# Kernel optimization log

Measured on AMD Instinct MI355X. Metric: run time of the kernel, lower is better.

The kernel has to match this reference:

```python
import jax, jax.numpy as jnp
import numpy as np

DIM = 768
HEADS = 12
HD = DIM // HEADS  # 64
WIN = 14
N = WIN * WIN  # 196
MLP_HID = 3072
EPS = 1e-6
SCALE = HD ** -0.5


def _ln(x, g, b):
    m = jnp.mean(x, axis=-1, keepdims=True)
    v = jnp.mean(jnp.square(x - m), axis=-1, keepdims=True)
    return (x - m) * jax.lax.rsqrt(v + EPS) * g + b


def _rel_table(rel):
    coords = jnp.arange(WIN)[:, None] - jnp.arange(WIN)[None, :] + (WIN - 1)
    return rel[coords]


def _window_partition(x, ws):
    B, H, W, C = x.shape
    pad_h = (ws - H % ws) % ws
    pad_w = (ws - W % ws) % ws
    x = jnp.pad(x, ((0, 0), (0, pad_h), (0, pad_w), (0, 0)))
    Hp, Wp = H + pad_h, W + pad_w
    x = x.reshape(B, Hp // ws, ws, Wp // ws, ws, C)
    win = x.transpose(0, 1, 3, 2, 4, 5).reshape(-1, ws, ws, C)
    return win, (Hp, Wp)


def _window_unpartition(win, ws, pad_hw, hw):
    Hp, Wp = pad_hw
    H, W = hw
    B = win.shape[0] // (Hp * Wp // ws // ws)
    x = win.reshape(B, Hp // ws, Wp // ws, ws, ws, -1)
    x = x.transpose(0, 1, 3, 2, 4, 5).reshape(B, Hp, Wp, -1)
    return x[:, :H, :W, :]


def _attention(x, qkv_w, qkv_b, proj_w, proj_b, rel_pos_h, rel_pos_w):
    Bw = x.shape[0]
    qkv = x.reshape(Bw, N, DIM) @ qkv_w + qkv_b  # (Bw, N, 3*DIM)
    qkv = qkv.reshape(Bw, N, 3, HEADS, HD).transpose(2, 0, 3, 1, 4)
    qkv = qkv.reshape(3, Bw * HEADS, N, HD)
    q, k, v = qkv[0], qkv[1], qkv[2]
    attn = jnp.einsum('bnd,bmd->bnm', q * SCALE, k)  # (Bw*H, N, N)
    Rh = _rel_table(rel_pos_h)
    Rw = _rel_table(rel_pos_w)
    r_q = q.reshape(-1, WIN, WIN, HD)
    rel_h = jnp.einsum('bhwc,hkc->bhwk', r_q, Rh)
    rel_w = jnp.einsum('bhwc,wkc->bhwk', r_q, Rw)
    attn = (attn.reshape(-1, WIN, WIN, WIN, WIN)
            + rel_h[:, :, :, :, None]
            + rel_w[:, :, :, None, :]).reshape(-1, N, N)
    attn = jax.nn.softmax(attn, axis=-1)
    out = jnp.einsum('bnm,bmd->bnd', attn, v)
    out = out.reshape(Bw, HEADS, WIN, WIN, HD).transpose(0, 2, 3, 1, 4)
    out = out.reshape(Bw, WIN, WIN, DIM)
    return out @ proj_w + proj_b


def setup_inputs() -> dict:
    key = jax.random.key(0)
    ks = jax.random.split(key, 10)
    s = 0.02
    return {
        'x': jax.random.normal(ks[0], (2, 64, 64, DIM), jnp.float32),
        'ln1_g': jnp.ones((DIM,), jnp.float32),
        'ln1_b': jnp.zeros((DIM,), jnp.float32),
        'qkv_w': jax.random.normal(ks[1], (DIM, 3 * DIM), jnp.float32) * s,
        'qkv_b': jax.random.normal(ks[2], (3 * DIM,), jnp.float32) * s,
        'proj_w': jax.random.normal(ks[3], (DIM, DIM), jnp.float32) * s,
        'proj_b': jax.random.normal(ks[4], (DIM,), jnp.float32) * s,
        'rel_pos_h': jax.random.normal(ks[5], (2 * WIN - 1, HD), jnp.float32) * s,
        'rel_pos_w': jax.random.normal(ks[6], (2 * WIN - 1, HD), jnp.float32) * s,
        'ln2_g': jnp.ones((DIM,), jnp.float32),
        'ln2_b': jnp.zeros((DIM,), jnp.float32),
        'fc1_w': jax.random.normal(ks[7], (DIM, MLP_HID), jnp.float32) * s,
        'fc1_b': jnp.zeros((MLP_HID,), jnp.float32),
        'fc2_w': jax.random.normal(ks[8], (MLP_HID, DIM), jnp.float32) * s,
        'fc2_b': jnp.zeros((DIM,), jnp.float32),
    }


def reference(x, ln1_g, ln1_b, qkv_w, qkv_b, proj_w, proj_b,
              rel_pos_h, rel_pos_w, ln2_g, ln2_b, fc1_w, fc1_b, fc2_w, fc2_b):
    B, H, W, _ = x.shape
    shortcut = x
    h = _ln(x, ln1_g, ln1_b)
    win, pad_hw = _window_partition(h, WIN)
    win = _attention(win, qkv_w, qkv_b, proj_w, proj_b, rel_pos_h, rel_pos_w)
    h = _window_unpartition(win, WIN, pad_hw, (H, W))
    x = shortcut + h  # drop_path prob 0 -> identity
    h = _ln(x, ln2_g, ln2_b)
    h = jax.nn.gelu(h @ fc1_w + fc1_b, approximate=False) @ fc2_w + fc2_b
    return x + h
```

## Files before the change

### kernel.cpp

```cpp
#include <hip/hip_runtime.h>
#include <hip/hip_bf16.h>
#include <math.h>


#define DIMC 768
#define HEADS 12
#define WIN 14
#define NTOK 196
#define NWIN 50
#define MROWS 9800
#define YROWS 8192
#define MLP_HID 3072

using bf16x8 = __attribute__((ext_vector_type(8))) short;
using f32x4  = __attribute__((ext_vector_type(4))) float;

__device__ __forceinline__ float bf2f(unsigned short u) {
    return __uint_as_float(((unsigned)u) << 16);
}
__device__ __forceinline__ unsigned short f2bf(float f) {
    unsigned u = __float_as_uint(f);
    unsigned r = (u + 0x7fffu + ((u >> 16) & 1u)) >> 16;
    return (unsigned short)r;
}
__device__ __forceinline__ void gl2lds16(const unsigned short* g, unsigned short* l) {
    __builtin_amdgcn_global_load_lds(
        (const __attribute__((address_space(1))) void*)g,
        (__attribute__((address_space(3))) void*)l, 16, 0, 0);
}

__device__ __forceinline__ float fast_gelu(float v) {
    float u = v * 0.70710678118654752f;
    float a = fabsf(u);
    float t = __builtin_amdgcn_rcpf(fmaf(0.3275911f, a, 1.0f));
    float p = t * fmaf(t, fmaf(t, fmaf(t, fmaf(t, 1.061405429f, -1.453152027f),
                       1.421413741f), -0.284496736f), 0.254829592f);
    float e = __expf(-u * u);
    float er = fmaf(-p, e, 1.0f);
    er = copysignf(er, v);
    return 0.5f * v * (1.0f + er);
}

__global__ __launch_bounds__(256) void transpose_all(
        const float* __restrict__ Wq, unsigned short* __restrict__ Tq,
        const float* __restrict__ Wp, unsigned short* __restrict__ Tp,
        const float* __restrict__ W1, unsigned short* __restrict__ T1,
        const float* __restrict__ W2, unsigned short* __restrict__ T2) {
    int id = blockIdx.x;
    const float* W; unsigned short* Wt; int K, N, nbx, rel;
    if (id < 432)       { W = Wq; Wt = Tq; K = 768;  N = 2304; nbx = 36; rel = id; }
    else if (id < 576)  { W = Wp; Wt = Tp; K = 768;  N = 768;  nbx = 12; rel = id - 432; }
    else if (id < 1152) { W = W1; Wt = T1; K = 768;  N = 3072; nbx = 48; rel = id - 576; }
    else                { W = W2; Wt = T2; K = 3072; N = 768;  nbx = 12; rel = id - 1152; }
    int bx = rel % nbx, by = rel / nbx;
    __shared__ float t[64][65];
    int k0 = by << 6, n0 = bx << 6;
    int tn = threadIdx.x & 63;
    int tk = threadIdx.x >> 6;
    #pragma unroll
    for (int r = 0; r < 16; r++) {
        int k = tk + r * 4;
        t[k][tn] = W[(size_t)(k0 + k) * N + n0 + tn];
    }
    __syncthreads();
    #pragma unroll
    for (int r = 0; r < 16; r++) {
        int n = tk + r * 4;
        Wt[(size_t)(n0 + n) * K + k0 + tn] = f2bf(t[tn][n]);
    }
}

__global__ __launch_bounds__(256) void ln1_win_kernel(
        const float* __restrict__ x, const float* __restrict__ g,
        const float* __restrict__ b, unsigned short* __restrict__ h1) {
    int tid = threadIdx.x;
    int row = blockIdx.x * 4 + (tid >> 6);
    int lane = tid & 63;
    if (row >= MROWS) return;
    int w = row / NTOK, t = row % NTOK;
    int bi = w / 25, wr = w % 25;
    int gy = (wr / 5) * WIN + t / WIN;
    int gx = (wr % 5) * WIN + t % WIN;
    unsigned short* out = h1 + (size_t)row * DIMC;
    if (gy >= 64 || gx >= 64) {
        #pragma unroll
        for (int j = 0; j < 12; j++) out[lane + 64 * j] = 0;
        return;
    }
    const float* xr = x + ((size_t)((bi * 64 + gy) * 64 + gx)) * DIMC;
    float v[12], s = 0.f;
    #pragma unroll
    for (int j = 0; j < 12; j++) { v[j] = xr[lane + 64 * j]; s += v[j]; }
    #pragma unroll
    for (int o = 32; o > 0; o >>= 1) s += __shfl_xor(s, o);
    float mean = s * (1.f / 768.f);
    float q = 0.f;
    #pragma unroll
    for (int j = 0; j < 12; j++) { float d = v[j] - mean; q += d * d; }
    #pragma unroll
    for (int o = 32; o > 0; o >>= 1) q += __shfl_xor(q, o);
    float inv = rsqrtf(q * (1.f / 768.f) + 1e-6f);
    #pragma unroll
    for (int j = 0; j < 12; j++) {
        int c = lane + 64 * j;
        out[c] = f2bf((v[j] - mean) * inv * g[c] + b[c]);
    }
}

__global__ __launch_bounds__(256) void ln2_kernel(
        const float* __restrict__ y, const float* __restrict__ g,
        const float* __restrict__ b, unsigned short* __restrict__ h2) {
    int tid = threadIdx.x;
    int row = blockIdx.x * 4 + (tid >> 6);
    int lane = tid & 63;
    const float* xr = y + (size_t)row * DIMC;
    float v[12], s = 0.f;
    #pragma unroll
    for (int j = 0; j < 12; j++) { v[j] = xr[lane + 64 * j]; s += v[j]; }
    #pragma unroll
    for (int o = 32; o > 0; o >>= 1) s += __shfl_xor(s, o);
    float mean = s * (1.f / 768.f);
    float q = 0.f;
    #pragma unroll
    for (int j = 0; j < 12; j++) { float d = v[j] - mean; q += d * d; }
    #pragma unroll
    for (int o = 32; o > 0; o >>= 1) q += __shfl_xor(q, o);
    float inv = rsqrtf(q * (1.f / 768.f) + 1e-6f);
    unsigned short* out = h2 + (size_t)row * DIMC;
    #pragma unroll
    for (int j = 0; j < 12; j++) {
        int c = lane + 64 * j;
        out[c] = f2bf((v[j] - mean) * inv * g[c] + b[c]);
    }
}

__global__ __launch_bounds__(256) void build_aug(
        const unsigned short* __restrict__ qkvb,
        const float* __restrict__ relph, const float* __restrict__ relpw,
        unsigned short* __restrict__ Aaug, unsigned short* __restrict__ Vt) {
    __shared__ unsigned short qs[208 * 72];
    __shared__ unsigned short rt[64 * 72];
    int tid = threadIdx.x;
    int bh = blockIdx.x, w = bh / HEADS, head = bh % HEADS;
    int lane = tid & 63, wave = tid >> 6;
    int l15 = lane & 15, q4 = lane >> 4, q8 = q4 * 8;
    size_t base = (size_t)w * NTOK * 2304 + head * 64;
    unsigned short* ab = Aaug + (size_t)bh * 256 * 96;

    for (int e = tid; e < 196 * 8; e += 256) {
        int t = e >> 3, s8 = (e & 7) * 8;
        bf16x8 qv = *(const bf16x8*)&qkvb[base + (size_t)t * 2304 + s8];
        *(bf16x8*)&qs[t * 72 + s8] = qv;
        *(bf16x8*)&ab[t * 96 + s8] = qv;
    }
    for (int e = tid; e < 12 * 8; e += 256) {
        bf16x8 z = {};
        *(bf16x8*)&qs[(196 + (e >> 3)) * 72 + (e & 7) * 8] = z;
    }
    for (int e = tid; e < 64 * 8; e += 256) {
        int r = e >> 3, s8 = (e & 7) * 8;
        bf16x8 ov = {};
        if (r < 54) {
            const float* src = (r < 27 ? relph + (size_t)r * 64
                                       : relpw + (size_t)(r - 27) * 64) + s8;
            #pragma unroll
            for (int jj = 0; jj < 8; jj++) ov[jj] = (short)f2bf(src[jj]);
        }
        *(bf16x8*)&rt[r * 72 + s8] = ov;
    }
    for (int e = tid; e < 60 * 12; e += 256) {
        bf16x8 z = {};
        *(bf16x8*)&ab[(size_t)(196 + e / 12) * 96 + (e % 12) * 8] = z;
    }
    for (int e = tid; e < 196; e += 256) {
        ab[e * 96 + 92] = 0; ab[e * 96 + 93] = 0;
        ab[e * 96 + 94] = 0; ab[e * 96 + 95] = 0;
    }
    __syncthreads();

    #pragma unroll
    for (int t = 0; t < 4; t++) {
        int it = wave * 4 + t;
        if (it >= 13) break;
        bf16x8 a0 = *(bf16x8*)&qs[(it * 16 + l15) * 72 + q8];
        bf16x8 a1 = *(bf16x8*)&qs[(it * 16 + l15) * 72 + 32 + q8];
        #pragma unroll
        for (int rt4 = 0; rt4 < 4; rt4++) {
            bf16x8 b0 = *(bf16x8*)&rt[(rt4 * 16 + l15) * 72 + q8];
            bf16x8 b1 = *(bf16x8*)&rt[(rt4 * 16 + l15) * 72 + 32 + q8];
            f32x4 d4 = {};
            d4 = __builtin_amdgcn_mfma_f32_16x16x32_bf16(a0, b0, d4, 0, 0, 0);
            d4 = __builtin_amdgcn_mfma_f32_16x16x32_bf16(a1, b1, d4, 0, 0, 0);
            int rcol = rt4 * 16 + l15;
            #pragma unroll
            for (int r = 0; r < 4; r++) {
                int i = it * 16 + q4 * 4 + r;
                if (i < 196 && rcol < 54) {
                    if (rcol < 27) {
                        int c = 13 + i / 14 - rcol;
                        if (c >= 0 && c < 14) ab[i * 96 + 64 + c] = f2bf(d4[r]);
                    } else {
                        int c = 13 + i % 14 - (rcol - 27);
                        if (c >= 0 && c < 14) ab[i * 96 + 78 + c] = f2bf(d4[r]);
                    }
                }
            }
        }
    }

    unsigned short* vtb = Vt + (size_t)bh * 64 * 224;
    for (int e = tid; e < 196 * 8; e += 256) {
        int j = e >> 3, dg = (e & 7) * 8;
        bf16x8 vv = *(const bf16x8*)&qkvb[base + 1536 + (size_t)j * 2304 + dg];
        #pragma unroll
        for (int k = 0; k < 8; k++)
            vtb[(size_t)(dg + k) * 224 + j] = (unsigned short)vv[k];
    }
    for (int e = tid; e < 64 * 28; e += 256)
        vtb[(size_t)(e / 28) * 224 + 196 + (e % 28)] = 0;
}

__global__ __launch_bounds__(256) void attn_mfma(
        const unsigned short* __restrict__ qkvb,
        const unsigned short* __restrict__ Aaug,
        const unsigned short* __restrict__ Vt,
        unsigned short* __restrict__ out) {
    __shared__ unsigned short Kls[208 * 96];
    __shared__ unsigned short Pls[4][64 * 40];
    int tid = threadIdx.x;
    int bh = blockIdx.x, w = bh / HEADS, head = bh % HEADS;
    int wave = tid >> 6, lane = tid & 63;
    int l15 = lane & 15, q4 = lane >> 4, q8 = q4 * 8;
    size_t kbase = (size_t)w * NTOK * 2304 + head * 64 + 768;
    for (int e = tid; e < 196 * 8; e += 256) {
        int t = e >> 3, s8 = (e & 7) * 8;
        bf16x8 kv = *(const bf16x8*)&qkvb[kbase + (size_t)t * 2304 + s8];
        bf16x8 ko;
        #pragma unroll
        for (int jj = 0; jj < 8; jj++)
            ko[jj] = (short)f2bf(bf2f((unsigned short)kv[jj]) * 0.125f);
        *(bf16x8*)&Kls[t * 96 + s8] = ko;
    }
    bf16x8 z8 = {};
    for (int e = tid; e < 208 * 4; e += 256)
        *(bf16x8*)&Kls[(e >> 2) * 96 + 64 + (e & 3) * 8] = z8;
    for (int e = tid; e < 12 * 8; e += 256)
        *(bf16x8*)&Kls[(196 + (e >> 3)) * 96 + (e & 7) * 8] = z8;
    __syncthreads();
    for (int e = tid; e < 196; e += 256) {
        Kls[e * 96 + 64 + e / WIN] = 0x3F80;
        Kls[e * 96 + 78 + e % WIN] = 0x3F80;
    }
    bf16x8 af[4][3];
    const unsigned short* abse = Aaug + (size_t)bh * 256 * 96;
    #pragma unroll
    for (int it = 0; it < 4; it++)
        #pragma unroll
        for (int c = 0; c < 3; c++)
            af[it][c] = *(const bf16x8*)&abse[(size_t)(wave * 64 + it * 16 + l15) * 96 + c * 32 + q8];
    __syncthreads();

    const unsigned short* vtb = Vt + (size_t)bh * 64 * 224;
    f32x4 o[4][4] = {};
    float lacc[4][4] = {{0.f}};
    bf16x8 bv[4];
    #pragma unroll
    for (int dt = 0; dt < 4; dt++)
        bv[dt] = *(const bf16x8*)&vtb[(dt * 16 + l15) * 224 + q8];

    for (int jp = 0; jp < 7; jp++) {
        f32x4 s[4][2] = {};
        #pragma unroll
        for (int half = 0; half < 2; half++) {
            int jt = jp * 2 + half;
            if (jt < 13) {
                #pragma unroll
                for (int c = 0; c < 3; c++) {
                    bf16x8 bk = *(bf16x8*)&Kls[(jt * 16 + l15) * 96 + c * 32 + q8];
                    #pragma unroll
                    for (int it = 0; it < 4; it++)
                        s[it][half] = __builtin_amdgcn_mfma_f32_16x16x32_bf16(
                            af[it][c], bk, s[it][half], 0, 0, 0);
                }
            }
        }
        __syncthreads();
        #pragma unroll
        for (int half = 0; half < 2; half++) {
            int jt = jp * 2 + half;
            bool valid = (jt < 13) && (jt * 16 + l15) < 196;
            #pragma unroll
            for (int it = 0; it < 4; it++)
                #pragma unroll
                for (int r = 0; r < 4; r++) {
                    float p = valid ? __expf(s[it][half][r]) : 0.f;
                    unsigned short pb = f2bf(p);
                    lacc[it][r] += bf2f(pb);
                    Pls[wave][(it * 16 + q4 * 4 + r) * 40 + half * 16 + l15] = pb;
                }
        }
        __syncthreads();
        bf16x8 ap[4];
        #pragma unroll
        for (int it = 0; it < 4; it++)
            ap[it] = *(bf16x8*)&Pls[wave][(it * 16 + l15) * 40 + q8];
        bf16x8 bvn[4];
        if (jp < 6) {
            #pragma unroll
            for (int dt = 0; dt < 4; dt++)
                bvn[dt] = *(const bf16x8*)&vtb[(dt * 16 + l15) * 224 + (jp + 1) * 32 + q8];
        }
        #pragma unroll
        for (int dt = 0; dt < 4; dt++)
            #pragma unroll
            for (int it = 0; it < 4; it++)
                o[it][dt] = __builtin_amdgcn_mfma_f32_16x16x32_bf16(
                    ap[it], bv[dt], o[it][dt], 0, 0, 0);
        if (jp < 6) {
            #pragma unroll
            for (int dt = 0; dt < 4; dt++) bv[dt] = bvn[dt];
        }
    }
    #pragma unroll
    for (int it = 0; it < 4; it++)
        #pragma unroll
        for (int r = 0; r < 4; r++) {
            float v = lacc[it][r];
            v += __shfl_xor(v, 1); v += __shfl_xor(v, 2);
            v += __shfl_xor(v, 4); v += __shfl_xor(v, 8);
            lacc[it][r] = 1.f / v;
        }
    #pragma unroll
    for (int it = 0; it < 4; it++) {
        int i0 = wave * 64 + it * 16 + q4 * 4;
        #pragma unroll
        for (int r = 0; r < 4; r++) {
            if (i0 + r < 196) {
                size_t rowb = (size_t)(w * NTOK + i0 + r) * DIMC + head * 64;
                #pragma unroll
                for (int dt = 0; dt < 4; dt++)
                    out[rowb + dt * 16 + l15] = f2bf(o[it][dt][r] * lacc[it][r]);
            }
        }
    }
}

template <int EPI, int BN>
__global__ __launch_bounds__(256) void mgemm(
        const unsigned short* __restrict__ A, const unsigned short* __restrict__ Bt,
        const float* __restrict__ bias, void* __restrict__ Cout,
        const float* __restrict__ resid, int M, int Nn, int K,
        int nbx, int nby) {
    const int NI = BN / 32;
    constexpr int LPT = (BN == 128) ? 4 : 3;
    __shared__ unsigned short As[3][128 * 32];
    __shared__ unsigned short Bs[3][BN * 32];
    int tid = threadIdx.x;
    int lane = tid & 63, wave = tid >> 6;
    int l15 = lane & 15, q4 = lane >> 4;
    int xq8 = (q4 ^ ((l15 >> 1) & 3)) * 8;
    int id = blockIdx.x;
    int per = nbx * 8;
    int s = id / per;
    int rem = id - s * per;
    int rmax = nby - s * 8; if (rmax > 8) rmax = 8;
    int bx = rem / rmax;
    int r_ = rem - bx * rmax;
    int by = s * 8 + r_;
    int m0 = by << 7, n0 = bx * BN;
    int wm = (wave >> 1) * 64, wn = (wave & 1) * (BN / 2);
    int srow0 = wave * 32 + (lane >> 2);
    int srow1 = srow0 + 16;
    int sseg = ((lane & 3) ^ ((lane >> 3) & 3)) * 8;
    int rmA0 = m0 + srow0; if (rmA0 >= M) rmA0 = M - 1;
    int rmA1 = m0 + srow1; if (rmA1 >= M) rmA1 = M - 1;
    const unsigned short* gA0 = A + (size_t)rmA0 * K + sseg;
    const unsigned short* gA1 = A + (size_t)rmA1 * K + sseg;
    int browB = (BN == 128) ? srow0 : (wave * 16 + (lane >> 2));
    const unsigned short* gB0 = Bt + (size_t)(n0 + browB) * K + sseg;
    const unsigned short* gB1 = Bt + (size_t)(n0 + srow1) * K + sseg;
    int lofsA = wave * 1024 + lane * 8;
    int lofsB = ((BN == 128) ? wave * 1024 : wave * 512) + lane * 8;
    f32x4 acc[4][NI] = {};
    int nt = K >> 5;
    gl2lds16(gA0, &As[0][lofsA]);
    gl2lds16(gA1, &As[0][lofsA + 512]);
    gl2lds16(gB0, &Bs[0][lofsB]);
    if (BN == 128) gl2lds16(gB1, &Bs[0][lofsB + 512]);
    if (nt > 1) {
        gl2lds16(gA0 + 32, &As[1][lofsA]);
        gl2lds16(gA1 + 32, &As[1][lofsA + 512]);
        gl2lds16(gB0 + 32, &Bs[1][lofsB]);
        if (BN == 128) gl2lds16(gB1 + 32, &Bs[1][lofsB + 512]);
    }
    int cur = 0;
    for (int t = 0; t < nt; ++t) {
        if (t + 1 < nt) {
            asm volatile("s_waitcnt vmcnt(%0)" :: "i"(LPT) : "memory");
        } else {
            asm volatile("s_waitcnt vmcnt(0)" ::: "memory");
        }
        __builtin_amdgcn_s_barrier();
        if (t + 2 < nt) {
            int b2 = cur + 2; if (b2 >= 3) b2 -= 3;
            int kn = (t + 2) << 5;
            gl2lds16(gA0 + kn, &As[b2][lofsA]);
            gl2lds16(gA1 + kn, &As[b2][lofsA + 512]);
            gl2lds16(gB0 + kn, &Bs[b2][lofsB]);
            if (BN == 128) gl2lds16(gB1 + kn, &Bs[b2][lofsB + 512]);
        }
        bf16x8 bfr[NI];
        #pragma unroll
        for (int ni = 0; ni < NI; ni++)
            bfr[ni] = *(bf16x8*)&Bs[cur][(wn + ni * 16 + l15) * 32 + xq8];
        #pragma unroll
        for (int mi = 0; mi < 4; mi++) {
            bf16x8 afr = *(bf16x8*)&As[cur][(wm + mi * 16 + l15) * 32 + xq8];
            #pragma unroll
            for (int ni = 0; ni < NI; ni++)
                acc[mi][ni] = __builtin_amdgcn_mfma_f32_16x16x32_bf16(
                    afr, bfr[ni], acc[mi][ni], 0, 0, 0);
        }
        cur = (cur == 2) ? 0 : cur + 1;
    }
    int q4r = (lane >> 4) * 4;
    #pragma unroll
    for (int mi = 0; mi < 4; mi++) {
        #pragma unroll
        for (int r = 0; r < 4; r++) {
            int row = m0 + wm + mi * 16 + q4r + r;
            if (row >= M) continue;
            if (EPI == 2) {
                int w = row / NTOK, t = row % NTOK;
                int bi = w / 25, wr = w % 25;
                int gy = (wr / 5) * WIN + t / WIN;
                int gx = (wr % 5) * WIN + t % WIN;
                if (gy >= 64 || gx >= 64) continue;
                size_t orow = ((size_t)((bi * 64 + gy) * 64 + gx)) * DIMC;
                #pragma unroll
                for (int ni = 0; ni < NI; ni++) {
                    int col = n0 + wn + ni * 16 + l15;
                    float v = acc[mi][ni][r] + bias[col];
                    ((float*)Cout)[orow + col] = resid[orow + col] + v;
                }
            } else {
                #pragma unroll
                for (int ni = 0; ni < NI; ni++) {
                    int col = n0 + wn + ni * 16 + l15;
                    float v = acc[mi][ni][r] + bias[col];
                    if (EPI == 0) {
                        ((unsigned short*)Cout)[(size_t)row * Nn + col] = f2bf(v);
                    } else if (EPI == 1) {
                        v = fast_gelu(v);
                        ((unsigned short*)Cout)[(size_t)row * Nn + col] = f2bf(v);
                    } else {
                        ((float*)Cout)[(size_t)row * Nn + col] =
                            resid[(size_t)row * Nn + col] + v;
                    }
                }
            }
        }
    }
}

extern "C" void kernel_launch(void* const* d_in, const int* in_sizes, int n_in,
                              void* d_out, int out_size, void* d_ws, size_t ws_size,
                              hipStream_t stream) {
    const float* x      = (const float*)d_in[0];
    const float* ln1_g  = (const float*)d_in[1];
    const float* ln1_b  = (const float*)d_in[2];
    const float* qkv_w  = (const float*)d_in[3];
    const float* qkv_b  = (const float*)d_in[4];
    const float* proj_w = (const float*)d_in[5];
    const float* proj_b = (const float*)d_in[6];
    const float* rel_h  = (const float*)d_in[7];
    const float* rel_w  = (const float*)d_in[8];
    const float* ln2_g  = (const float*)d_in[9];
    const float* ln2_b  = (const float*)d_in[10];
    const float* fc1_w  = (const float*)d_in[11];
    const float* fc1_b  = (const float*)d_in[12];
    const float* fc2_w  = (const float*)d_in[13];
    const float* fc2_b  = (const float*)d_in[14];
    float* out = (float*)d_out;
    char* ws = (char*)d_ws;

    unsigned short* wt_qkv  = (unsigned short*)(ws);
    unsigned short* wt_proj = (unsigned short*)(ws + 3538944);
    unsigned short* wt_fc1  = (unsigned short*)(ws + 4718592);
    unsigned short* wt_fc2  = (unsigned short*)(ws + 9437184);
    unsigned short* qkvb    = (unsigned short*)(ws + 14155776);
    float*          yb      = (float*)        (ws + 14155776);
    unsigned short* h2      = (unsigned short*)(ws + 39321600);
    unsigned short* h1      = (unsigned short*)(ws + 59314176);
    unsigned short* attn_o  = h1;
    unsigned short* zb      = h1;
    unsigned short* Aaug    = (unsigned short*)(ws + 74366976);
    unsigned short* Vt      = (unsigned short*)(ws + 103858176);

    transpose_all<<<1728, 256, 0, stream>>>(
        qkv_w, wt_qkv, proj_w, wt_proj, fc1_w, wt_fc1, fc2_w, wt_fc2);

    ln1_win_kernel<<<(MROWS + 3) / 4, 256, 0, stream>>>(x, ln1_g, ln1_b, h1);

    mgemm<0, 128><<<18 * 77, 256, 0, stream>>>(
        h1, wt_qkv, qkv_b, qkvb, nullptr, MROWS, 2304, DIMC, 18, 77);

    build_aug<<<NWIN * HEADS, 256, 0, stream>>>(qkvb, rel_h, rel_w, Aaug, Vt);

    attn_mfma<<<NWIN * HEADS, 256, 0, stream>>>(qkvb, Aaug, Vt, attn_o);

    mgemm<2, 64><<<12 * 77, 256, 0, stream>>>(
        attn_o, wt_proj, proj_b, yb, x, MROWS, DIMC, DIMC, 12, 77);

    ln2_kernel<<<YROWS / 4, 256, 0, stream>>>(yb, ln2_g, ln2_b, h2);

    mgemm<1, 128><<<24 * 64, 256, 0, stream>>>(
        h2, wt_fc1, fc1_b, zb, nullptr, YROWS, MLP_HID, DIMC, 24, 64);

    mgemm<3, 64><<<12 * 64, 256, 0, stream>>>(
        zb, wt_fc2, fc2_b, out, yb, YROWS, DIMC, MLP_HID, 12, 64);
}
```

Baseline: 428.7 us.

## Add 256x256-tile 8-wave GEMM with phased LDS prefetch for QKV and FC1

Introduces a new 512-thread GEMM kernel using 256x256 output tiles, with double-buffered LDS split into K-halves and direct global-to-LDS loads interleaved with MFMA phases. It also adds grouped block swizzling for L2 locality. QKV and FC1 projections now use it, which raises data reuse per tile and overlaps loads with compute. The cost is larger LDS (128KB) and higher register use, which lower occupancy, plus partial-tile waste when M=9800.

Measured after the change: 543.5 us. +26.8%, slower.

```diff
diff --git a/kernel.cpp b/kernel.cpp
--- a/kernel.cpp
+++ b/kernel.cpp
@@ -340,6 +340,128 @@
                 #pragma unroll
                 for (int dt = 0; dt < 4; dt++)
                     out[rowb + dt * 16 + l15] = f2bf(o[it][dt][r] * lacc[it][r]);
+            }
+        }
+    }
+}
+
+template <int EPI>
+__global__ __launch_bounds__(512) void mgemm8(
+        const unsigned short* __restrict__ A, const unsigned short* __restrict__ Bt,
+        const float* __restrict__ bias, void* __restrict__ Cout,
+        int M, int Nn, int K, int nbx, int nby) {
+    __shared__ unsigned short AsF[2 * 2 * 8192];
+    __shared__ unsigned short BsF[2 * 2 * 8192];
+    int tid = threadIdx.x;
+    int lane = tid & 63, wave = tid >> 6;
+    int l15 = lane & 15, q4 = lane >> 4;
+    int id = blockIdx.x;
+    int per = nbx * 8;
+    int s = id / per;
+    int rem = id - s * per;
+    int rmax = nby - s * 8; if (rmax > 8) rmax = 8;
+    int bx = rem / rmax;
+    int r_ = rem - bx * rmax;
+    int by = s * 8 + r_;
+    int m0 = by << 8, n0 = bx << 8;
+    int wm = (wave >> 2) << 7;
+    int wn = (wave & 3) << 6;
+    int fseg = (q4 ^ ((l15 >> 1) & 3)) * 8;
+    int pa[8], pb[4];
+    #pragma unroll
+    for (int i = 0; i < 8; i++) pa[i] = (wm + i * 16 + l15) * 32 + fseg;
+    #pragma unroll
+    for (int i = 0; i < 4; i++) pb[i] = (wn + i * 16 + l15) * 32 + fseg;
+    int srow = tid >> 2;
+    int sseg = ((tid & 3) ^ ((tid >> 3) & 3)) * 8;
+    int ra0 = m0 + srow;        if (ra0 >= M) ra0 = M - 1;
+    int ra1 = m0 + 128 + srow;  if (ra1 >= M) ra1 = M - 1;
+    const unsigned short* gA0 = A + (size_t)ra0 * K + sseg;
+    const unsigned short* gA1 = A + (size_t)ra1 * K + sseg;
+    const unsigned short* gB0 = Bt + (size_t)(n0 + srow) * K + sseg;
+    const unsigned short* gB1 = Bt + (size_t)(n0 + 128 + srow) * K + sseg;
+    int ld = tid * 8;
+    f32x4 acc[8][4] = {};
+    int NT = K >> 6;
+    gl2lds16(gA0,      &AsF[ld]);        gl2lds16(gA1,      &AsF[4096 + ld]);
+    gl2lds16(gB0,      &BsF[ld]);        gl2lds16(gB1,      &BsF[4096 + ld]);
+    gl2lds16(gA0 + 32, &AsF[8192 + ld]); gl2lds16(gA1 + 32, &AsF[8192 + 4096 + ld]);
+    gl2lds16(gB0 + 32, &BsF[8192 + ld]); gl2lds16(gB1 + 32, &BsF[8192 + 4096 + ld]);
+    asm volatile("s_waitcnt vmcnt(0)" ::: "memory");
+    __builtin_amdgcn_s_barrier();
+
+#define MG8_PHASE(Q)                                                          \
+    {                                                                         \
+        constexpr int h = (Q) >> 1, m2 = (Q) & 1;                             \
+        int hb = ((t & 1) * 2 + h) * 8192;                                    \
+        bf16x8 af0 = *(bf16x8*)&AsF[hb + pa[m2 * 4 + 0]];                     \
+        bf16x8 af1 = *(bf16x8*)&AsF[hb + pa[m2 * 4 + 1]];                     \
+        bf16x8 af2 = *(bf16x8*)&AsF[hb + pa[m2 * 4 + 2]];                     \
+        bf16x8 af3 = *(bf16x8*)&AsF[hb + pa[m2 * 4 + 3]];                     \
+        bf16x8 bf0 = *(bf16x8*)&BsF[hb + pb[0]];                              \
+        bf16x8 bf1 = *(bf16x8*)&BsF[hb + pb[1]];                              \
+        bf16x8 bf2 = *(bf16x8*)&BsF[hb + pb[2]];                              \
+        bf16x8 bf3 = *(bf16x8*)&BsF[hb + pb[3]];                              \
+        if (t + 1 < NT) {                                                     \
+            int hb2 = (((t + 1) & 1) * 2 + h) * 8192;                         \
+            int go = (t + 1) * 64 + h * 32;                                   \
+            if ((Q) & 1) {                                                    \
+                gl2lds16(gB0 + go, &BsF[hb2 + ld]);                           \
+                gl2lds16(gB1 + go, &BsF[hb2 + 4096 + ld]);                    \
+            } else {                                                          \
+                gl2lds16(gA0 + go, &AsF[hb2 + ld]);                           \
+                gl2lds16(gA1 + go, &AsF[hb2 + 4096 + ld]);                    \
+            }                                                                 \
+        }                                                                     \
+        if ((Q) & 1) {                                                        \
+            if (t + 1 < NT) asm volatile("s_waitcnt vmcnt(4)" ::: "memory");  \
+            else            asm volatile("s_waitcnt vmcnt(0)" ::: "memory");  \
+        }                                                                     \
+        __builtin_amdgcn_sched_barrier(0);                                    \
+        __builtin_amdgcn_s_barrier();                                         \
+        __builtin_amdgcn_s_setprio(1);                                        \
+        acc[m2*4+0][0] = __builtin_amdgcn_mfma_f32_16x16x32_bf16(af0, bf0, acc[m2*4+0][0], 0, 0, 0); \
+        acc[m2*4+0][1] = __builtin_amdgcn_mfma_f32_16x16x32_bf16(af0, bf1, acc[m2*4+0][1], 0, 0, 0); \
+        acc[m2*4+0][2] = __builtin_amdgcn_mfma_f32_16x16x32_bf16(af0, bf2, acc[m2*4+0][2], 0, 0, 0); \
+        acc[m2*4+0][3] = __builtin_amdgcn_mfma_f32_16x16x32_bf16(af0, bf3, acc[m2*4+0][3], 0, 0, 0); \
+        acc[m2*4+1][0] = __builtin_amdgcn_mfma_f32_16x16x32_bf16(af1, bf0, acc[m2*4+1][0], 0, 0, 0); \
+        acc[m2*4+1][1] = __builtin_amdgcn_mfma_f32_16x16x32_bf16(af1, bf1, acc[m2*4+1][1], 0, 0, 0); \
+        acc[m2*4+1][2] = __builtin_amdgcn_mfma_f32_16x16x32_bf16(af1, bf2, acc[m2*4+1][2], 0, 0, 0); \
+        acc[m2*4+1][3] = __builtin_amdgcn_mfma_f32_16x16x32_bf16(af1, bf3, acc[m2*4+1][3], 0, 0, 0); \
+        acc[m2*4+2][0] = __builtin_amdgcn_mfma_f32_16x16x32_bf16(af2, bf0, acc[m2*4+2][0], 0, 0, 0); \
+        acc[m2*4+2][1] = __builtin_amdgcn_mfma_f32_16x16x32_bf16(af2, bf1, acc[m2*4+2][1], 0, 0, 0); \
+        acc[m2*4+2][2] = __builtin_amdgcn_mfma_f32_16x16x32_bf16(af2, bf2, acc[m2*4+2][2], 0, 0, 0); \
+        acc[m2*4+2][3] = __builtin_amdgcn_mfma_f32_16x16x32_bf16(af2, bf3, acc[m2*4+2][3], 0, 0, 0); \
+        acc[m2*4+3][0] = __builtin_amdgcn_mfma_f32_16x16x32_bf16(af3, bf0, acc[m2*4+3][0], 0, 0, 0); \
+        acc[m2*4+3][1] = __builtin_amdgcn_mfma_f32_16x16x32_bf16(af3, bf1, acc[m2*4+3][1], 0, 0, 0); \
+        acc[m2*4+3][2] = __builtin_amdgcn_mfma_f32_16x16x32_bf16(af3, bf2, acc[m2*4+3][2], 0, 0, 0); \
+        acc[m2*4+3][3] = __builtin_amdgcn_mfma_f32_16x16x32_bf16(af3, bf3, acc[m2*4+3][3], 0, 0, 0); \
+        __builtin_amdgcn_s_setprio(0);                                        \
+        __builtin_amdgcn_sched_barrier(0);                                    \
+        __builtin_amdgcn_s_barrier();                                         \
+    }
+
+    for (int t = 0; t < NT; ++t) {
+        MG8_PHASE(0)
+        MG8_PHASE(1)
+        MG8_PHASE(2)
+        MG8_PHASE(3)
+    }
+#undef MG8_PHASE
+
+    int q4r = q4 * 4;
+    #pragma unroll
+    for (int mi = 0; mi < 8; mi++) {
+        #pragma unroll
+        for (int r = 0; r < 4; r++) {
+            int row = m0 + wm + mi * 16 + q4r + r;
+            if (row >= M) continue;
+            #pragma unroll
+            for (int ni = 0; ni < 4; ni++) {
+                int col = n0 + wn + ni * 16 + l15;
+                float v = acc[mi][ni][r] + bias[col];
+                if (EPI == 1) v = fast_gelu(v);
+                ((unsigned short*)Cout)[(size_t)row * Nn + col] = f2bf(v);
             }
         }
     }
@@ -448,15 +570,8 @@
                 for (int ni = 0; ni < NI; ni++) {
                     int col = n0 + wn + ni * 16 + l15;
                     float v = acc[mi][ni][r] + bias[col];
-                    if (EPI == 0) {
-                        ((unsigned short*)Cout)[(size_t)row * Nn + col] = f2bf(v);
-                    } else if (EPI == 1) {
-                        v = fast_gelu(v);
-                        ((unsigned short*)Cout)[(size_t)row * Nn + col] = f2bf(v);
-                    } else {
-                        ((float*)Cout)[(size_t)row * Nn + col] =
-                            resid[(size_t)row * Nn + col] + v;
-                    }
+                    ((float*)Cout)[(size_t)row * Nn + col] =
+                        resid[(size_t)row * Nn + col] + v;
                 }
             }
         }
@@ -502,8 +617,8 @@
 
     ln1_win_kernel<<<(MROWS + 3) / 4, 256, 0, stream>>>(x, ln1_g, ln1_b, h1);
 
-    mgemm<0, 128><<<18 * 77, 256, 0, stream>>>(
-        h1, wt_qkv, qkv_b, qkvb, nullptr, MROWS, 2304, DIMC, 18, 77);
+    mgemm8<0><<<9 * 39, 512, 0, stream>>>(
+        h1, wt_qkv, qkv_b, qkvb, MROWS, 2304, DIMC, 9, 39);
 
     build_aug<<<NWIN * HEADS, 256, 0, stream>>>(qkvb, rel_h, rel_w, Aaug, Vt);
 
@@ -514,8 +629,8 @@
 
     ln2_kernel<<<YROWS / 4, 256, 0, stream>>>(yb, ln2_g, ln2_b, h2);
 
-    mgemm<1, 128><<<24 * 64, 256, 0, stream>>>(
-        h2, wt_fc1, fc1_b, zb, nullptr, YROWS, MLP_HID, DIMC, 24, 64);
+    mgemm8<1><<<12 * 32, 512, 0, stream>>>(
+        h2, wt_fc1, fc1_b, zb, YROWS, MLP_HID, DIMC, 12, 32);
 
     mgemm<3, 64><<<12 * 64, 256, 0, stream>>>(
         zb, wt_fc2, fc2_b, out, yb, YROWS, DIMC, MLP_HID, 12, 64);
```

## Add relative-position bias via LDS lookup instead of augmented QK GEMM

Applied to the files above, without the earlier changes.

Before, the relative-position terms were folded into the QK^T product by padding Q to 96 columns with scattered rel dots and adding one-hot columns to K. Now build_aug writes only the compact q·R dot table (208x56 per head), and attn_mfma loads Q straight from qkvb, runs a 64-wide QK GEMM, and adds the two bias terms per score through LDS lookups with division-by-14 index math. This cuts one third of the QK MFMAs and the bytes of the augmented Q buffer. The cost is extra per-element LDS reads and integer work inside the softmax loop.

Result: slower. 456.9 us (+6.6%).

```diff
diff --git a/kernel.cpp b/kernel.cpp
--- a/kernel.cpp
+++ b/kernel.cpp
@@ -137,7 +137,7 @@
 __global__ __launch_bounds__(256) void build_aug(
         const unsigned short* __restrict__ qkvb,
         const float* __restrict__ relph, const float* __restrict__ relpw,
-        unsigned short* __restrict__ Aaug, unsigned short* __restrict__ Vt) {
+        unsigned short* __restrict__ dots_g, unsigned short* __restrict__ Vt) {
     __shared__ unsigned short qs[208 * 72];
     __shared__ unsigned short rt[64 * 72];
     int tid = threadIdx.x;
@@ -145,13 +145,11 @@
     int lane = tid & 63, wave = tid >> 6;
     int l15 = lane & 15, q4 = lane >> 4, q8 = q4 * 8;
     size_t base = (size_t)w * NTOK * 2304 + head * 64;
-    unsigned short* ab = Aaug + (size_t)bh * 256 * 96;
 
     for (int e = tid; e < 196 * 8; e += 256) {
         int t = e >> 3, s8 = (e & 7) * 8;
         bf16x8 qv = *(const bf16x8*)&qkvb[base + (size_t)t * 2304 + s8];
         *(bf16x8*)&qs[t * 72 + s8] = qv;
-        *(bf16x8*)&ab[t * 96 + s8] = qv;
     }
     for (int e = tid; e < 12 * 8; e += 256) {
         bf16x8 z = {};
@@ -168,16 +166,9 @@
         }
         *(bf16x8*)&rt[r * 72 + s8] = ov;
     }
-    for (int e = tid; e < 60 * 12; e += 256) {
-        bf16x8 z = {};
-        *(bf16x8*)&ab[(size_t)(196 + e / 12) * 96 + (e % 12) * 8] = z;
-    }
-    for (int e = tid; e < 196; e += 256) {
-        ab[e * 96 + 92] = 0; ab[e * 96 + 93] = 0;
-        ab[e * 96 + 94] = 0; ab[e * 96 + 95] = 0;
-    }
     __syncthreads();
 
+    unsigned short* db = dots_g + (size_t)bh * 208 * 56;
     #pragma unroll
     for (int t = 0; t < 4; t++) {
         int it = wave * 4 + t;
@@ -195,15 +186,9 @@
             #pragma unroll
             for (int r = 0; r < 4; r++) {
                 int i = it * 16 + q4 * 4 + r;
-                if (i < 196 && rcol < 54) {
-                    if (rcol < 27) {
-                        int c = 13 + i / 14 - rcol;
-                        if (c >= 0 && c < 14) ab[i * 96 + 64 + c] = f2bf(d4[r]);
-                    } else {
-                        int c = 13 + i % 14 - (rcol - 27);
-                        if (c >= 0 && c < 14) ab[i * 96 + 78 + c] = f2bf(d4[r]);
-                    }
-                }
+                if (rcol < 56)
+                    db[i * 56 + rcol] =
+                        (i < 196 && rcol < 54) ? f2bf(d4[r]) : (unsigned short)0;
             }
         }
     }
@@ -222,16 +207,18 @@
 
 __global__ __launch_bounds__(256) void attn_mfma(
         const unsigned short* __restrict__ qkvb,
-        const unsigned short* __restrict__ Aaug,
+        const unsigned short* __restrict__ dots_g,
         const unsigned short* __restrict__ Vt,
         unsigned short* __restrict__ out) {
-    __shared__ unsigned short Kls[208 * 96];
+    __shared__ unsigned short Kls[208 * 72];
+    __shared__ unsigned short Dls[208 * 56];
     __shared__ unsigned short Pls[4][64 * 40];
     int tid = threadIdx.x;
     int bh = blockIdx.x, w = bh / HEADS, head = bh % HEADS;
     int wave = tid >> 6, lane = tid & 63;
     int l15 = lane & 15, q4 = lane >> 4, q8 = q4 * 8;
-    size_t kbase = (size_t)w * NTOK * 2304 + head * 64 + 768;
+    size_t qbase = (size_t)w * NTOK * 2304 + head * 64;
+    size_t kbase = qbase + 768;
     for (int e = tid; e < 196 * 8; e += 256) {
         int t = e >> 3, s8 = (e & 7) * 8;
         bf16x8 kv = *(const bf16x8*)&qkvb[kbase + (size_t)t * 2304 + s8];
@@ -239,25 +226,27 @@
         #pragma unroll
         for (int jj = 0; jj < 8; jj++)
             ko[jj] = (short)f2bf(bf2f((unsigned short)kv[jj]) * 0.125f);
-        *(bf16x8*)&Kls[t * 96 + s8] = ko;
+        *(bf16x8*)&Kls[t * 72 + s8] = ko;
     }
     bf16x8 z8 = {};
-    for (int e = tid; e < 208 * 4; e += 256)
-        *(bf16x8*)&Kls[(e >> 2) * 96 + 64 + (e & 3) * 8] = z8;
     for (int e = tid; e < 12 * 8; e += 256)
-        *(bf16x8*)&Kls[(196 + (e >> 3)) * 96 + (e & 7) * 8] = z8;
-    __syncthreads();
-    for (int e = tid; e < 196; e += 256) {
-        Kls[e * 96 + 64 + e / WIN] = 0x3F80;
-        Kls[e * 96 + 78 + e % WIN] = 0x3F80;
-    }
-    bf16x8 af[4][3];
-    const unsigned short* abse = Aaug + (size_t)bh * 256 * 96;
-    #pragma unroll
-    for (int it = 0; it < 4; it++)
-        #pragma unroll
-        for (int c = 0; c < 3; c++)
-            af[it][c] = *(const bf16x8*)&abse[(size_t)(wave * 64 + it * 16 + l15) * 96 + c * 32 + q8];
+        *(bf16x8*)&Kls[(196 + (e >> 3)) * 72 + (e & 7) * 8] = z8;
+    {
+        const unsigned short* dg = dots_g + (size_t)bh * 208 * 56;
+        for (int e = tid; e < 208 * 7; e += 256) {
+            int row = e / 7, ch = e - row * 7;
+            *(bf16x8*)&Dls[row * 56 + ch * 8] = *(const bf16x8*)&dg[row * 56 + ch * 8];
+        }
+    }
+    bf16x8 af[4][2];
+    #pragma unroll
+    for (int it = 0; it < 4; it++) {
+        int arow = wave * 64 + it * 16 + l15;
+        if (arow > 195) arow = 195;
+        #pragma unroll
+        for (int c = 0; c < 2; c++)
+            af[it][c] = *(const bf16x8*)&qkvb[qbase + (size_t)arow * 2304 + c * 32 + q8];
+    }
     __syncthreads();
 
     const unsigned short* vtb = Vt + (size_t)bh * 64 * 224;
@@ -275,8 +264,8 @@
             int jt = jp * 2 + half;
             if (jt < 13) {
                 #pragma unroll
-                for (int c = 0; c < 3; c++) {
-                    bf16x8 bk = *(bf16x8*)&Kls[(jt * 16 + l15) * 96 + c * 32 + q8];
+                for (int c = 0; c < 2; c++) {
+                    bf16x8 bk = *(bf16x8*)&Kls[(jt * 16 + l15) * 72 + c * 32 + q8];
                     #pragma unroll
                     for (int it = 0; it < 4; it++)
                         s[it][half] = __builtin_amdgcn_mfma_f32_16x16x32_bf16(
@@ -288,12 +277,21 @@
         #pragma unroll
         for (int half = 0; half < 2; half++) {
             int jt = jp * 2 + half;
-            bool valid = (jt < 13) && (jt * 16 + l15) < 196;
+            int j = jt * 16 + l15;
+            bool valid = (jt < 13) && (j < 196);
+            int jd = (j * 4682) >> 16;
+            int jm = j - 14 * jd;
             #pragma unroll
             for (int it = 0; it < 4; it++)
                 #pragma unroll
                 for (int r = 0; r < 4; r++) {
-                    float p = valid ? __expf(s[it][half][r]) : 0.f;
+                    int i = it * 16 + q4 * 4 + r;
+                    int ii = (i > 195) ? 195 : i;
+                    int iid = (ii * 4682) >> 16;
+                    int iim = ii - 14 * iid;
+                    float rel = bf2f(Dls[ii * 56 + 13 + iid - jd])
+                              + bf2f(Dls[ii * 56 + 40 + iim - jm]);
+                    float p = valid ? __expf(s[it][half][r] + rel) : 0.f;
                     unsigned short pb = f2bf(p);
                     lacc[it][r] += bf2f(pb);
                     Pls[wave][(it * 16 + q4 * 4 + r) * 40 + half * 16 + l15] = pb;
@@ -494,7 +492,7 @@
     unsigned short* h1      = (unsigned short*)(ws + 59314176);
     unsigned short* attn_o  = h1;
     unsigned short* zb      = h1;
-    unsigned short* Aaug    = (unsigned short*)(ws + 74366976);
+    unsigned short* dots_g  = (unsigned short*)(ws + 74366976);
     unsigned short* Vt      = (unsigned short*)(ws + 103858176);
 
     transpose_all<<<1728, 256, 0, stream>>>(
@@ -505,9 +503,9 @@
     mgemm<0, 128><<<18 * 77, 256, 0, stream>>>(
         h1, wt_qkv, qkv_b, qkvb, nullptr, MROWS, 2304, DIMC, 18, 77);
 
-    build_aug<<<NWIN * HEADS, 256, 0, stream>>>(qkvb, rel_h, rel_w, Aaug, Vt);
-
-    attn_mfma<<<NWIN * HEADS, 256, 0, stream>>>(qkvb, Aaug, Vt, attn_o);
+    build_aug<<<NWIN * HEADS, 256, 0, stream>>>(qkvb, rel_h, rel_w, dots_g, Vt);
+
+    attn_mfma<<<NWIN * HEADS, 256, 0, stream>>>(qkvb, dots_g, Vt, attn_o);
 
     mgemm<2, 64><<<12 * 77, 256, 0, stream>>>(
         attn_o, wt_proj, proj_b, yb, x, MROWS, DIMC, DIMC, 12, 77);
```

## Move softmax scale into Q, load K via direct global-to-LDS with XOR swizzle

Applied to the files above, without the earlier changes.

The 1/8 attention scale is now folded into the Q copy in build_aug, so attn_mfma can load K with raw gl2lds16 direct global-to-LDS copies into an XOR-swizzled 64-wide buffer, and the one-hot relative-position columns move into a separate Koh buffer. The per-iteration block barriers around the per-wave P buffer become a wave-local lgkmcnt wait, and the P row stride is padded from 40 to 44. This is meant to cut VALU conversion work, LDS bank conflicts and barrier stalls. It relies on P being wave-private. The padded stride may break the alignment of the 16-byte P reads, and the extra bf16 rounding of scaled Q slightly changes numerics.

New measurement: 415.3 us. 1.03x faster.

```diff
diff --git a/kernel.cpp b/kernel.cpp
--- a/kernel.cpp
+++ b/kernel.cpp
@@ -151,7 +151,11 @@
         int t = e >> 3, s8 = (e & 7) * 8;
         bf16x8 qv = *(const bf16x8*)&qkvb[base + (size_t)t * 2304 + s8];
         *(bf16x8*)&qs[t * 72 + s8] = qv;
-        *(bf16x8*)&ab[t * 96 + s8] = qv;
+        bf16x8 qo;
+        #pragma unroll
+        for (int jj = 0; jj < 8; jj++)
+            qo[jj] = (short)f2bf(bf2f((unsigned short)qv[jj]) * 0.125f);
+        *(bf16x8*)&ab[t * 96 + s8] = qo;
     }
     for (int e = tid; e < 12 * 8; e += 256) {
         bf16x8 z = {};
@@ -225,31 +229,30 @@
         const unsigned short* __restrict__ Aaug,
         const unsigned short* __restrict__ Vt,
         unsigned short* __restrict__ out) {
-    __shared__ unsigned short Kls[208 * 96];
-    __shared__ unsigned short Pls[4][64 * 40];
+    __shared__ unsigned short Kk[208 * 64];
+    __shared__ unsigned short Koh[208 * 40];
+    __shared__ unsigned short Pls[4][64 * 44];
     int tid = threadIdx.x;
     int bh = blockIdx.x, w = bh / HEADS, head = bh % HEADS;
     int wave = tid >> 6, lane = tid & 63;
     int l15 = lane & 15, q4 = lane >> 4, q8 = q4 * 8;
     size_t kbase = (size_t)w * NTOK * 2304 + head * 64 + 768;
-    for (int e = tid; e < 196 * 8; e += 256) {
-        int t = e >> 3, s8 = (e & 7) * 8;
-        bf16x8 kv = *(const bf16x8*)&qkvb[kbase + (size_t)t * 2304 + s8];
-        bf16x8 ko;
-        #pragma unroll
-        for (int jj = 0; jj < 8; jj++)
-            ko[jj] = (short)f2bf(bf2f((unsigned short)kv[jj]) * 0.125f);
-        *(bf16x8*)&Kls[t * 96 + s8] = ko;
+    {
+        int sw = ((lane & 7) ^ (lane >> 3)) * 8;
+        for (int r0 = wave * 8; r0 < 208; r0 += 32) {
+            int grow = r0 + (lane >> 3);
+            if (grow > 195) grow = 195;
+            gl2lds16(&qkvb[kbase + (size_t)grow * 2304 + sw],
+                     &Kk[r0 * 64 + lane * 8]);
+        }
     }
     bf16x8 z8 = {};
-    for (int e = tid; e < 208 * 4; e += 256)
-        *(bf16x8*)&Kls[(e >> 2) * 96 + 64 + (e & 3) * 8] = z8;
-    for (int e = tid; e < 12 * 8; e += 256)
-        *(bf16x8*)&Kls[(196 + (e >> 3)) * 96 + (e & 7) * 8] = z8;
+    for (int e = tid; e < 208 * 5; e += 256)
+        *(bf16x8*)&Koh[(e / 5) * 40 + (e % 5) * 8] = z8;
     __syncthreads();
     for (int e = tid; e < 196; e += 256) {
-        Kls[e * 96 + 64 + e / WIN] = 0x3F80;
-        Kls[e * 96 + 78 + e % WIN] = 0x3F80;
+        Koh[e * 40 + e / WIN] = 0x3F80;
+        Koh[e * 40 + 14 + e % WIN] = 0x3F80;
     }
     bf16x8 af[4][3];
     const unsigned short* abse = Aaug + (size_t)bh * 256 * 96;
@@ -274,17 +277,22 @@
         for (int half = 0; half < 2; half++) {
             int jt = jp * 2 + half;
             if (jt < 13) {
+                int krow = jt * 16 + l15;
                 #pragma unroll
-                for (int c = 0; c < 3; c++) {
-                    bf16x8 bk = *(bf16x8*)&Kls[(jt * 16 + l15) * 96 + c * 32 + q8];
+                for (int c = 0; c < 2; c++) {
+                    bf16x8 bk = *(bf16x8*)&Kk[krow * 64 + (((c * 4 + q4) ^ (l15 & 7)) * 8)];
                     #pragma unroll
                     for (int it = 0; it < 4; it++)
                         s[it][half] = __builtin_amdgcn_mfma_f32_16x16x32_bf16(
                             af[it][c], bk, s[it][half], 0, 0, 0);
                 }
+                bf16x8 bo = *(bf16x8*)&Koh[krow * 40 + q8];
+                #pragma unroll
+                for (int it = 0; it < 4; it++)
+                    s[it][half] = __builtin_amdgcn_mfma_f32_16x16x32_bf16(
+                        af[it][2], bo, s[it][half], 0, 0, 0);
             }
         }
-        __syncthreads();
         #pragma unroll
         for (int half = 0; half < 2; half++) {
             int jt = jp * 2 + half;
@@ -296,14 +304,14 @@
                     float p = valid ? __expf(s[it][half][r]) : 0.f;
                     unsigned short pb = f2bf(p);
                     lacc[it][r] += bf2f(pb);
-                    Pls[wave][(it * 16 + q4 * 4 + r) * 40 + half * 16 + l15] = pb;
+                    Pls[wave][(it * 16 + q4 * 4 + r) * 44 + half * 16 + l15] = pb;
                 }
         }
-        __syncthreads();
+        asm volatile("s_waitcnt lgkmcnt(0)" ::: "memory");
         bf16x8 ap[4];
         #pragma unroll
         for (int it = 0; it < 4; it++)
-            ap[it] = *(bf16x8*)&Pls[wave][(it * 16 + l15) * 40 + q8];
+            ap[it] = *(bf16x8*)&Pls[wave][(it * 16 + l15) * 44 + q8];
         bf16x8 bvn[4];
         if (jp < 6) {
             #pragma unroll
```
